# Kernel optimization log

Measured on AMD Instinct MI355X. Metric: run time of the kernel, lower is better.

Reference implementation:

```python
import jax, jax.numpy as jnp
import numpy as np

# Production-scale dims (see shape_source)
B = 8            # batch size
P = 32768        # points per sample
Q = 2048         # supernodes per sample
N = B * P        # 262144 total points
S = B * Q        # 16384 total supernodes
MAX_DEG = 32
E = S * MAX_DEG  # 524288 edges
IN_DIM = 16
H = 192          # hidden_dim, divisible by ndim=3, per-dim 64 (even) -> no padding
NDIM = 3
MAX_WAVELENGTH = 10000.0


def sincos_embed(pos):
    # ContinuousSincosEmbed: dim split evenly over ndim, sin/cos halves per coord
    dpn = H // NDIM                                                   # 64
    omega = 1.0 / MAX_WAVELENGTH ** (jnp.arange(0, dpn, 2, dtype=jnp.float32) / dpn)  # [dpn/2]
    out = pos[..., None] * omega                                      # [N, ndim, dpn/2]
    emb = jnp.concatenate([jnp.sin(out), jnp.cos(out)], axis=-1)      # [N, ndim, dpn]
    return emb.reshape(pos.shape[0], H)                               # [N, H]


def setup_inputs() -> dict:
    key = jax.random.key(0)
    ks = jax.random.split(key, 8)
    input_feat = jax.random.normal(ks[0], (N, IN_DIM), jnp.float32)
    input_pos = jax.random.uniform(ks[1], (N, NDIM), jnp.float32) * 100.0
    batch_idx = jnp.repeat(jnp.arange(B, dtype=jnp.int32), P)
    # Q supernodes per sample, globally sorted & unique (as from radius_graph filter)
    ar = jnp.arange(S, dtype=jnp.int32)
    supernode_idxs = (ar // Q) * P + (ar % Q)
    # edges: each supernode is dst of MAX_DEG edges; src within same sample
    dst_idx = jnp.repeat(supernode_idxs, MAX_DEG)
    src_idx = (dst_idx // P) * P + jax.random.randint(ks[2], (E,), 0, P, dtype=jnp.int32)
    # params (LinearProjection = affine)
    W_in = jax.random.normal(ks[3], (IN_DIM, H), jnp.float32) / np.sqrt(IN_DIM)
    b_in = jnp.zeros((H,), jnp.float32)
    W1 = jax.random.normal(ks[4], (2 * H, H), jnp.float32) / np.sqrt(2 * H)
    b1 = jnp.zeros((H,), jnp.float32)
    W2 = jax.random.normal(ks[5], (H, H), jnp.float32) / np.sqrt(H)
    b2 = jnp.zeros((H,), jnp.float32)
    return {"input_feat": input_feat, "input_pos": input_pos,
            "supernode_idxs": supernode_idxs, "batch_idx": batch_idx,
            "src_idx": src_idx, "dst_idx": dst_idx,
            "W_in": W_in, "b_in": b_in, "W1": W1, "b1": b1, "W2": W2, "b2": b2}


def reference(input_feat, input_pos, supernode_idxs, batch_idx, src_idx, dst_idx,
              W_in, b_in, W1, b1, W2, b2):
    # x = input_proj(feat) + pos_embed(pos)        [N, H]
    x = input_feat @ W_in + b_in + sincos_embed(input_pos)
    # gather src/dst node features per edge, concat  [E, 2H]
    m = jnp.concatenate([x[src_idx], x[dst_idx]], axis=1)
    # message MLP: Linear -> GELU(exact) -> Linear   [E, H]
    m = jax.nn.gelu(m @ W1 + b1, approximate=False) @ W2 + b2
    # segment-mean by destination supernode (segment_csr 'mean' equivalent)
    seg = jnp.searchsorted(supernode_idxs, dst_idx)  # [E] in [0, S)
    sums = jax.ops.segment_sum(m, seg, num_segments=S)
    cnt = jax.ops.segment_sum(jnp.ones((E,), m.dtype), seg, num_segments=S)
    pooled = sums / cnt[:, None]                     # [S, H]
    return pooled.reshape(B, S // B, H)              # [B, Q, H]
```

## Files before the change

kernel.cpp:

```cpp
#include <hip/hip_runtime.h>
#include <hip/hip_bf16.h>


#define HD 192
#define INF 16
#define N_NODES 262144
#define N_SUP 16384
#define ROWB 384

typedef __attribute__((ext_vector_type(8))) short bf16x8;
typedef __attribute__((ext_vector_type(4))) float f32x4;

__device__ __forceinline__ unsigned f2bf(float f) {
    unsigned x = __float_as_uint(f);
    return (x + 0x7fffu + ((x >> 16) & 1u)) >> 16;
}
__device__ __forceinline__ float bf2f(unsigned short u) {
    return __uint_as_float(((unsigned)u) << 16);
}
__device__ __forceinline__ void gload16(const void* g, void* l) {
    __builtin_amdgcn_global_load_lds(
        (const __attribute__((address_space(1))) unsigned int*)g,
        (__attribute__((address_space(3))) unsigned int*)l, 16, 0, 0);
}
__device__ __forceinline__ void gelu_acc(float v, float& acc) {
    const float m   = v * fmaf(v * v, -0.1029392f, -2.3021178f);
    const float den = 1.f + exp2f(m);
    const float r   = __builtin_amdgcn_rcpf(den);
    acc = fmaf(v, r, acc);
}

__global__ void prep_kernel(const float* __restrict__ W1,
                            const float* __restrict__ Win,
                            unsigned short* __restrict__ Wt,
                            unsigned short* __restrict__ Wb,
                            float* __restrict__ Wint)
{
    const int i = blockIdx.x * 256 + threadIdx.x;
    if (i < 36864) {
        const int n = i / HD, k = i % HD;
        Wt[i] = (unsigned short)f2bf(W1[k * HD + n]);
    } else if (i < 73728) {
        const int j = i - 36864;
        const int n = j / HD, k = j % HD;
        Wb[j] = (unsigned short)f2bf(W1[(size_t)(HD + k) * HD + n]);
    } else if (i < 76800) {
        const int j = i - 73728;
        const int c = j / INF, k = j % INF;
        Wint[j] = Win[k * HD + c];
    }
}

__global__ __launch_bounds__(256, 2)
void xcomp_kernel(const float* __restrict__ feat,
                  const float* __restrict__ pos,
                  const float* __restrict__ Wint,
                  const float* __restrict__ bin,
                  unsigned short* __restrict__ xswz)
{
    __shared__ __align__(16) float feat_s[4][256];
    __shared__ float pos_s[4][48];
    __shared__ __align__(16) unsigned short dstg[4][16 * HD];

    const int t = threadIdx.x, w = t >> 6, l = t & 63;

    float win[3][INF];
    #pragma unroll
    for (int d = 0; d < 3; ++d)
        #pragma unroll
        for (int q = 0; q < 4; ++q)
            *reinterpret_cast<float4*>(&win[d][q * 4]) =
                *reinterpret_cast<const float4*>(Wint + (size_t)(l + 64 * d) * INF + q * 4);
    float bcol[3];
    #pragma unroll
    for (int d = 0; d < 3; ++d) bcol[d] = bin[l + 64 * d];
    const float om = exp2f(-(float)(l & 31) * 0.41524101186098287f);
    const float phase = (l < 32) ? 0.f : 1.57079632679f;

    for (int gg = 0; gg < 4; ++gg) {
        const int row0 = blockIdx.x * 256 + gg * 64 + w * 16;

        {
            const float4 f4 = *reinterpret_cast<const float4*>(
                feat + (size_t)(row0 + (l >> 2)) * INF + (l & 3) * 4);
            *reinterpret_cast<float4*>(&feat_s[w][(l >> 2) * 16 + (l & 3) * 4]) = f4;
            if (l < 48) pos_s[w][l] = pos[(size_t)row0 * 3 + l];
        }

        for (int r = 0; r < 16; ++r) {
            float fr[INF];
            #pragma unroll
            for (int q = 0; q < 4; ++q)
                *reinterpret_cast<float4*>(&fr[q * 4]) =
                    *reinterpret_cast<const float4*>(&feat_s[w][r * 16 + q * 4]);
            #pragma unroll
            for (int d = 0; d < 3; ++d) {
                const float pe = __sinf(fmaf(pos_s[w][r * 3 + d], om, phase));
                float acc = bcol[d] + pe;
                #pragma unroll
                for (int k = 0; k < INF; ++k) acc = fmaf(fr[k], win[d][k], acc);
                dstg[w][r * HD + l + 64 * d] = (unsigned short)f2bf(acc);
            }
        }

        #pragma unroll
        for (int q = 0; q < 6; ++q) {
            const int id = q * 64 + l;
            const int rl = id / 24, c = id % 24;
            const bf16x8 v = *reinterpret_cast<const bf16x8*>(&dstg[w][rl * HD + c * 8]);
            *reinterpret_cast<bf16x8*>((char*)xswz +
                (size_t)(row0 + rl) * ROWB + ((c ^ (rl & 7)) * 16)) = v;
        }
    }
}

template<bool GATHER>
__global__ __launch_bounds__(256, 2)
void agemm_kernel(const unsigned short* __restrict__ xswz,
                  const int* __restrict__ gidx,
                  const unsigned short* __restrict__ Wt,
                  const float* __restrict__ bias,
                  unsigned short* __restrict__ outp,
                  const int out_stride,
                  const int ntiles)
{
    __shared__ __align__(16) unsigned short xbuf[2][64 * HD];
    __shared__ int nid[64];

    const int t = threadIdx.x, w = t >> 6, l = t & 63;

    bf16x8 bfr[3][6];
    #pragma unroll
    for (int ct = 0; ct < 3; ++ct) {
        const int col = w * 48 + ct * 16 + (l & 15);
        const unsigned short* wp = Wt + (size_t)col * HD + (l >> 4) * 8;
        #pragma unroll
        for (int ks = 0; ks < 6; ++ks)
            bfr[ct][ks] = *reinterpret_cast<const bf16x8*>(wp + ks * 32);
    }
    float bias_c[3] = {0.f, 0.f, 0.f};
    if (GATHER) {
        #pragma unroll
        for (int ct = 0; ct < 3; ++ct) bias_c[ct] = bias[w * 48 + ct * 16 + (l & 15)];
        if (t < 64) nid[t] = gidx[blockIdx.x * 64 + t];
        __syncthreads();
    }

    auto STAGE = [&](int tile, int buf) {
        char* lbase = (char*)&xbuf[buf][0];
        if constexpr (GATHER) {
            #pragma unroll
            for (int i = 0; i < 6; ++i) {
                const int slot = w * 64 + i * 256 + l;
                const int r = slot / 24, p = slot % 24;
                const int node = nid[r];
                const char* src = (const char*)xswz + (size_t)node * ROWB +
                                  (((p ^ (r & 7)) ^ (node & 7)) * 16);
                gload16(src, lbase + w * 1024 + i * 4096);
            }
        } else {
            const char* gb = (const char*)xswz +
                             (size_t)(blockIdx.x * ntiles + tile) * 64 * ROWB;
            #pragma unroll
            for (int i = 0; i < 6; ++i)
                gload16(gb + w * 1024 + i * 4096 + l * 16, lbase + w * 1024 + i * 4096);
        }
    };

    STAGE(0, 0);
    __syncthreads();

    for (int tt = 0; tt < ntiles; ++tt) {
        const int cur = tt & 1;
        if (tt + 1 < ntiles) STAGE(tt + 1, cur ^ 1);

        f32x4 acc[4][3];
        #pragma unroll
        for (int rt = 0; rt < 4; ++rt)
            #pragma unroll
            for (int ct = 0; ct < 3; ++ct)
                acc[rt][ct] = (f32x4){0.f, 0.f, 0.f, 0.f};

        const char* xb = (const char*)&xbuf[cur][0];
        #pragma unroll
        for (int ks = 0; ks < 6; ++ks) {
            bf16x8 af[4];
            #pragma unroll
            for (int rt = 0; rt < 4; ++rt) {
                const int row = rt * 16 + (l & 15);
                const int p = (ks * 4 + (l >> 4)) ^ (l & 7);
                af[rt] = *reinterpret_cast<const bf16x8*>(xb + row * ROWB + p * 16);
            }
            #pragma unroll
            for (int rt = 0; rt < 4; ++rt)
                #pragma unroll
                for (int ct = 0; ct < 3; ++ct)
                    acc[rt][ct] = __builtin_amdgcn_mfma_f32_16x16x32_bf16(
                        af[rt], bfr[ct][ks], acc[rt][ct], 0, 0, 0);
        }
        __syncthreads();

        char* db = (char*)&xbuf[cur][0];
        #pragma unroll
        for (int rt = 0; rt < 4; ++rt)
            #pragma unroll
            for (int ct = 0; ct < 3; ++ct) {
                const int col = w * 48 + ct * 16 + (l & 15);
                const int ch = col >> 3, off = col & 7;
                #pragma unroll
                for (int j = 0; j < 4; ++j) {
                    const int row = rt * 16 + (l >> 4) * 4 + j;
                    *reinterpret_cast<unsigned short*>(
                        db + row * ROWB + ((ch ^ (row & 7)) * 16) + off * 2) =
                        (unsigned short)f2bf(acc[rt][ct][j] + bias_c[ct]);
                }
            }
        const size_t orow0 = GATHER ? (size_t)blockIdx.x * 64
                                    : (size_t)(blockIdx.x * ntiles + tt) * 64;
        #pragma unroll
        for (int q = 0; q < 6; ++q) {
            const int id = q * 64 + l;
            const int rid = id / 6, cc = id % 6;
            const int c = w * 6 + cc;
            const bf16x8 v = *reinterpret_cast<const bf16x8*>(
                db + rid * ROWB + ((c ^ (rid & 7)) * 16));
            *reinterpret_cast<bf16x8*>(outp + (orow0 + rid) * out_stride + c * 8) = v;
        }
        __syncthreads();
    }
}

__global__ __launch_bounds__(192)
void pool_kernel(const unsigned short* __restrict__ a,
                 const unsigned short* __restrict__ bC,
                 const int* __restrict__ src_idx,
                 float* __restrict__ g)
{
    __shared__ int sA[128];
    const int t = threadIdx.x;
    if (t < 128) sA[t] = src_idx[(size_t)blockIdx.x * 128 + t] * ROWB;
    __syncthreads();

    const int sl = t / 48;
    const int c4 = t % 48;
    const size_t s = (size_t)blockIdx.x * 4 + sl;
    const int* sp = sA + sl * 32;
    const int cb = c4 * 8;

    const ushort4 bu = *reinterpret_cast<const ushort4*>(bC + s * 384 + c4 * 4);
    const float b0 = bf2f(bu.x), b1v = bf2f(bu.y), b2v = bf2f(bu.z), b3v = bf2f(bu.w);

    const char* ab = (const char*)a;
    float a0 = 0.f, a1 = 0.f, a2 = 0.f, a3 = 0.f;
    #pragma unroll
    for (int e0 = 0; e0 < 32; e0 += 8) {
        uint2 u[8];
        #pragma unroll
        for (int i = 0; i < 8; ++i)
            u[i] = *reinterpret_cast<const uint2*>(ab + (size_t)(unsigned)(sp[e0 + i] + cb));
        #pragma unroll
        for (int i = 0; i < 8; ++i) {
            gelu_acc(__uint_as_float(u[i].x << 16)          + b0,  a0);
            gelu_acc(__uint_as_float(u[i].x & 0xffff0000u)  + b1v, a1);
            gelu_acc(__uint_as_float(u[i].y << 16)          + b2v, a2);
            gelu_acc(__uint_as_float(u[i].y & 0xffff0000u)  + b3v, a3);
        }
    }
    __syncthreads();
    float4 r;
    r.x = a0 * 0.03125f; r.y = a1 * 0.03125f; r.z = a2 * 0.03125f; r.w = a3 * 0.03125f;
    *reinterpret_cast<float4*>(g + s * HD + c4 * 4) = r;
}

__global__ __launch_bounds__(256, 2)
void gemm192_kernel(const float* __restrict__ A,
                    const float* __restrict__ W,
                    const float* __restrict__ bias,
                    float* __restrict__ out)
{
    __shared__ float xsf[64][196];
    __shared__ float wchunk[32][HD];
    const int t    = threadIdx.x;
    const int row0 = blockIdx.x * 64;

    const float4* ap = reinterpret_cast<const float4*>(A + (size_t)row0 * HD);
    #pragma unroll
    for (int q = 0; q < 12; ++q) {
        const int f4 = t + q * 256;
        const int r = f4 / 48, c = f4 % 48;
        *reinterpret_cast<float4*>(&xsf[r][c * 4]) = ap[f4];
    }

    const int tr = t >> 4;
    const int tc = t & 15;
    float acc[4][12];
    #pragma unroll
    for (int i = 0; i < 4; ++i)
        #pragma unroll
        for (int j = 0; j < 12; ++j) acc[i][j] = 0.f;

    for (int kc = 0; kc < 6; ++kc) {
        __syncthreads();
        {
            const float4* wp = reinterpret_cast<const float4*>(W + kc * 32 * HD);
            float4* wsp = reinterpret_cast<float4*>(&wchunk[0][0]);
            #pragma unroll
            for (int q = 0; q < 6; ++q) wsp[t + q * 256] = wp[t + q * 256];
        }
        __syncthreads();
        #pragma unroll 4
        for (int k = 0; k < 32; ++k) {
            const int kg = kc * 32 + k;
            float xv[4];
            #pragma unroll
            for (int i = 0; i < 4; ++i) xv[i] = xsf[tr * 4 + i][kg];
            float wv[12];
            #pragma unroll
            for (int j4 = 0; j4 < 3; ++j4)
                *reinterpret_cast<float4*>(&wv[j4 * 4]) =
                    *reinterpret_cast<const float4*>(&wchunk[k][tc * 12 + j4 * 4]);
            #pragma unroll
            for (int i = 0; i < 4; ++i)
                #pragma unroll
                for (int j = 0; j < 12; ++j)
                    acc[i][j] = fmaf(xv[i], wv[j], acc[i][j]);
        }
    }

    float bb[12];
    #pragma unroll
    for (int j = 0; j < 12; ++j) bb[j] = bias[tc * 12 + j];

    #pragma unroll
    for (int i = 0; i < 4; ++i) {
        float* o = out + (size_t)(row0 + tr * 4 + i) * HD + tc * 12;
        #pragma unroll
        for (int j4 = 0; j4 < 3; ++j4) {
            float4 v;
            v.x = acc[i][j4 * 4 + 0] + bb[j4 * 4 + 0];
            v.y = acc[i][j4 * 4 + 1] + bb[j4 * 4 + 1];
            v.z = acc[i][j4 * 4 + 2] + bb[j4 * 4 + 2];
            v.w = acc[i][j4 * 4 + 3] + bb[j4 * 4 + 3];
            *reinterpret_cast<float4*>(o + j4 * 4) = v;
        }
    }
}

extern "C" void kernel_launch(void* const* d_in, const int* in_sizes, int n_in,
                              void* d_out, int out_size, void* d_ws, size_t ws_size,
                              hipStream_t stream)
{
    const float* feat = (const float*)d_in[0];
    const float* pos  = (const float*)d_in[1];
    const int*   sup  = (const int*)d_in[2];
    const int*   src  = (const int*)d_in[4];
    const float* Win  = (const float*)d_in[6];
    const float* bin  = (const float*)d_in[7];
    const float* W1   = (const float*)d_in[8];
    const float* b1   = (const float*)d_in[9];
    const float* W2   = (const float*)d_in[10];
    const float* b2   = (const float*)d_in[11];

    char* ws = (char*)d_ws;
    unsigned short* Wt   = (unsigned short*)ws;
    unsigned short* Wb   = (unsigned short*)(ws + 73728);
    float*          Wint = (float*)(ws + 147456);
    unsigned short* x    = (unsigned short*)(ws + 159744);
    char*           C    = ws + 159744 + 100663296;
    float* out = (float*)d_out;

    prep_kernel<<<300, 256, 0, stream>>>(W1, Win, Wt, Wb, Wint);
    xcomp_kernel<<<N_NODES / 256, 256, 0, stream>>>(feat, pos, Wint, bin, x);
    agemm_kernel<true><<<N_SUP / 64, 256, 0, stream>>>(
        x, sup, Wb, b1, (unsigned short*)C, 384, 1);
    agemm_kernel<false><<<N_NODES / 256, 256, 0, stream>>>(
        x, nullptr, Wt, nullptr, x, HD, 4);
    pool_kernel<<<N_SUP / 4, 192, 0, stream>>>(x, (const unsigned short*)C, src, (float*)C);
    gemm192_kernel<<<N_SUP / 64, 256, 0, stream>>>((const float*)C, W2, b2, out);
}
```

Before: 254.3 us.

## Fuse source-side W1 projection into per-edge pooling with MFMA

The separate pass that projected every node through the source half of W1 and wrote the result back over x is removed. The new pooling kernel gathers the raw bf16 x rows for each edge into double-buffered LDS, multiplies them by W1 with MFMA, adds the destination-side bias, applies GELU and reduces to the segment mean. This saves a full read and write of the large node feature array and one kernel launch. In exchange it roughly doubles the matmul work, because it runs per edge instead of per node.

```diff
diff --git a/kernel.cpp b/kernel.cpp
--- a/kernel.cpp
+++ b/kernel.cpp
@@ -7,6 +7,7 @@
 #define N_NODES 262144
 #define N_SUP 16384
 #define ROWB 384
+#define EP_TILES 4
 
 typedef __attribute__((ext_vector_type(8))) short bf16x8;
 typedef __attribute__((ext_vector_type(4))) float f32x4;
@@ -230,46 +231,99 @@
     }
 }
 
-__global__ __launch_bounds__(192)
-void pool_kernel(const unsigned short* __restrict__ a,
-                 const unsigned short* __restrict__ bC,
-                 const int* __restrict__ src_idx,
-                 float* __restrict__ g)
-{
-    __shared__ int sA[128];
-    const int t = threadIdx.x;
-    if (t < 128) sA[t] = src_idx[(size_t)blockIdx.x * 128 + t] * ROWB;
+__global__ __launch_bounds__(256, 2)
+void edgepool_kernel(const unsigned short* __restrict__ xswz,
+                     const int* __restrict__ src_idx,
+                     const unsigned short* __restrict__ Wt,
+                     const unsigned short* __restrict__ bC,
+                     float* __restrict__ g)
+{
+    __shared__ __align__(16) unsigned short xbuf[2][64 * HD];
+
+    const int t = threadIdx.x, w = t >> 6, l = t & 63;
+
+    bf16x8 bfr[3][6];
+    #pragma unroll
+    for (int ct = 0; ct < 3; ++ct) {
+        const int col = w * 48 + ct * 16 + (l & 15);
+        const unsigned short* wp = Wt + (size_t)col * HD + (l >> 4) * 8;
+        #pragma unroll
+        for (int ks = 0; ks < 6; ++ks)
+            bfr[ct][ks] = *reinterpret_cast<const bf16x8*>(wp + ks * 32);
+    }
+
+    auto STAGE = [&](int tile, int buf) {
+        char* lbase = (char*)&xbuf[buf][0] + w * 1024;
+        const int* se = src_idx + (size_t)(blockIdx.x * EP_TILES + tile) * 64;
+        #pragma unroll
+        for (int i = 0; i < 6; ++i) {
+            const int slot = w * 64 + i * 256 + l;
+            const int r = slot / 24, p = slot % 24;
+            const int node = se[r];
+            const char* src = (const char*)xswz + (size_t)node * ROWB +
+                              (((p ^ (r & 7)) ^ (node & 7)) * 16);
+            gload16(src, lbase + i * 4096);
+        }
+    };
+
+    STAGE(0, 0);
     __syncthreads();
 
-    const int sl = t / 48;
-    const int c4 = t % 48;
-    const size_t s = (size_t)blockIdx.x * 4 + sl;
-    const int* sp = sA + sl * 32;
-    const int cb = c4 * 8;
-
-    const ushort4 bu = *reinterpret_cast<const ushort4*>(bC + s * 384 + c4 * 4);
-    const float b0 = bf2f(bu.x), b1v = bf2f(bu.y), b2v = bf2f(bu.z), b3v = bf2f(bu.w);
-
-    const char* ab = (const char*)a;
-    float a0 = 0.f, a1 = 0.f, a2 = 0.f, a3 = 0.f;
-    #pragma unroll
-    for (int e0 = 0; e0 < 32; e0 += 8) {
-        uint2 u[8];
-        #pragma unroll
-        for (int i = 0; i < 8; ++i)
-            u[i] = *reinterpret_cast<const uint2*>(ab + (size_t)(unsigned)(sp[e0 + i] + cb));
-        #pragma unroll
-        for (int i = 0; i < 8; ++i) {
-            gelu_acc(__uint_as_float(u[i].x << 16)          + b0,  a0);
-            gelu_acc(__uint_as_float(u[i].x & 0xffff0000u)  + b1v, a1);
-            gelu_acc(__uint_as_float(u[i].y << 16)          + b2v, a2);
-            gelu_acc(__uint_as_float(u[i].y & 0xffff0000u)  + b3v, a3);
-        }
-    }
-    __syncthreads();
-    float4 r;
-    r.x = a0 * 0.03125f; r.y = a1 * 0.03125f; r.z = a2 * 0.03125f; r.w = a3 * 0.03125f;
-    *reinterpret_cast<float4*>(g + s * HD + c4 * 4) = r;
+    for (int tt = 0; tt < EP_TILES; ++tt) {
+        const int cur = tt & 1;
+        if (tt + 1 < EP_TILES) STAGE(tt + 1, cur ^ 1);
+
+        f32x4 acc[4][3];
+        #pragma unroll
+        for (int rt = 0; rt < 4; ++rt)
+            #pragma unroll
+            for (int ct = 0; ct < 3; ++ct)
+                acc[rt][ct] = (f32x4){0.f, 0.f, 0.f, 0.f};
+
+        const char* xb = (const char*)&xbuf[cur][0];
+        #pragma unroll
+        for (int ks = 0; ks < 6; ++ks) {
+            bf16x8 af[4];
+            #pragma unroll
+            for (int rt = 0; rt < 4; ++rt) {
+                const int row = rt * 16 + (l & 15);
+                const int p = (ks * 4 + (l >> 4)) ^ (l & 7);
+                af[rt] = *reinterpret_cast<const bf16x8*>(xb + row * ROWB + p * 16);
+            }
+            #pragma unroll
+            for (int rt = 0; rt < 4; ++rt)
+                #pragma unroll
+                for (int ct = 0; ct < 3; ++ct)
+                    acc[rt][ct] = __builtin_amdgcn_mfma_f32_16x16x32_bf16(
+                        af[rt], bfr[ct][ks], acc[rt][ct], 0, 0, 0);
+        }
+
+        const size_t s0 = (size_t)(blockIdx.x * EP_TILES + tt) * 2;
+        float bval[2][3];
+        #pragma unroll
+        for (int sn = 0; sn < 2; ++sn)
+            #pragma unroll
+            for (int ct = 0; ct < 3; ++ct)
+                bval[sn][ct] = bf2f(bC[(s0 + sn) * 384 + w * 48 + ct * 16 + (l & 15)]);
+
+        __syncthreads();
+
+        #pragma unroll
+        for (int sn = 0; sn < 2; ++sn)
+            #pragma unroll
+            for (int ct = 0; ct < 3; ++ct) {
+                float part = 0.f;
+                #pragma unroll
+                for (int rr = 0; rr < 2; ++rr)
+                    #pragma unroll
+                    for (int j = 0; j < 4; ++j)
+                        gelu_acc(acc[sn * 2 + rr][ct][j] + bval[sn][ct], part);
+                part += __shfl_xor(part, 16);
+                part += __shfl_xor(part, 32);
+                if (l < 16)
+                    g[(s0 + sn) * HD + w * 48 + ct * 16 + l] = part * 0.03125f;
+            }
+    }
 }
 
 __global__ __launch_bounds__(256, 2)
@@ -373,8 +427,7 @@
     xcomp_kernel<<<N_NODES / 256, 256, 0, stream>>>(feat, pos, Wint, bin, x);
     agemm_kernel<true><<<N_SUP / 64, 256, 0, stream>>>(
         x, sup, Wb, b1, (unsigned short*)C, 384, 1);
-    agemm_kernel<false><<<N_NODES / 256, 256, 0, stream>>>(
-        x, nullptr, Wt, nullptr, x, HD, 4);
-    pool_kernel<<<N_SUP / 4, 192, 0, stream>>>(x, (const unsigned short*)C, src, (float*)C);
+    edgepool_kernel<<<N_SUP / (2 * EP_TILES), 256, 0, stream>>>(
+        x, src, Wt, (const unsigned short*)C, (float*)C);
     gemm192_kernel<<<N_SUP / 64, 256, 0, stream>>>((const float*)C, W2, b2, out);
 }
```

After: 248.9 us. 2.1% less time.
